# Performance work log

Hardware: AMD Instinct MI355X
Metric: run time of the kernel (lower is better)

Reference implementation:

```python
import jax, jax.numpy as jnp
import numpy as np

N_NODES = 10000
NEG_SLOPE = 0.2  # PyG GATv2Conv default


def gatv2(x, src, dst, Wl, bl, Wr, br, att, bias, n_nodes):
    """Single-head GATv2Conv (PyG defaults: heads=1, concat=True, self-loops added by caller)."""
    xl = x @ Wl + bl            # [N, dout] message source transform (lin_l)
    xr = x @ Wr + br            # [N, dout] target transform (lin_r)
    h = jax.nn.leaky_relu(xl[src] + xr[dst], NEG_SLOPE)   # [E, dout]
    e = h @ att                                            # [E] attention logits
    m = jax.ops.segment_max(e, dst, num_segments=n_nodes)  # per-target max
    ex = jnp.exp(e - m[dst])
    s = jax.ops.segment_sum(ex, dst, num_segments=n_nodes)
    alpha = ex / s[dst]                                    # segment softmax over incoming edges
    out = jax.ops.segment_sum(alpha[:, None] * xl[src], dst, num_segments=n_nodes)
    return out + bias


def _glorot(key, shape, scale=0.05):
    return jax.random.normal(key, shape, dtype=jnp.float32) * scale


def setup_inputs() -> dict:
    key = jax.random.key(0)
    ks = jax.random.split(key, 20)
    d_in, d0, d1 = 1000, 256, 128
    E = 320000
    x = jax.random.normal(ks[0], (N_NODES, d_in), dtype=jnp.float32)
    edge_index = jax.random.randint(ks[1], (2, E), 0, N_NODES, dtype=jnp.int64)
    return {
        "x": x,
        "edge_index": edge_index,
        # proj_in: d_in -> 256
        "Wpi": _glorot(ks[2], (d_in, d0)), "bpi": jnp.zeros((d0,), jnp.float32),
        # enc GATv2Conv 256 -> 128
        "Wl1": _glorot(ks[3], (d0, d1)), "bl1": jnp.zeros((d1,), jnp.float32),
        "Wr1": _glorot(ks[4], (d0, d1)), "br1": jnp.zeros((d1,), jnp.float32),
        "att1": _glorot(ks[5], (d1,)), "bias1": jnp.zeros((d1,), jnp.float32),
        # dec GATv2Conv 128 -> 256
        "Wl2": _glorot(ks[6], (d1, d0)), "bl2": jnp.zeros((d0,), jnp.float32),
        "Wr2": _glorot(ks[7], (d1, d0)), "br2": jnp.zeros((d0,), jnp.float32),
        "att2": _glorot(ks[8], (d0,)), "bias2": jnp.zeros((d0,), jnp.float32),
        # proj_out: 256 -> d_in
        "Wpo": _glorot(ks[9], (d0, d_in)), "bpo": jnp.zeros((d_in,), jnp.float32),
    }


def reference(x, edge_index, Wpi, bpi, Wl1, bl1, Wr1, br1, att1, bias1,
              Wl2, bl2, Wr2, br2, att2, bias2, Wpo, bpo):
    n = x.shape[0]
    # add self-loops (PyG GATv2Conv default add_self_loops=True)
    loops = jnp.arange(n, dtype=edge_index.dtype)
    src = jnp.concatenate([edge_index[0], loops])
    dst = jnp.concatenate([edge_index[1], loops])
    h = x @ Wpi + bpi
    z = gatv2(h, src, dst, Wl1, bl1, Wr1, br1, att1, bias1, n)
    d = gatv2(z, src, dst, Wl2, bl2, Wr2, br2, att2, bias2, n)
    x_hat = d @ Wpo + bpo
    return (x_hat, z)
```

## Files before the change

### kernel.cpp

```cpp
#include <hip/hip_runtime.h>
#include <math.h>

#define N_NODES 10000
#define MPAD    10112
#define D_IN    1000
#define KPAD_IN 1024
#define D0      256
#define D1      128
#define NPAD_OUT 1024
#define NEG_SLOPE 0.2f

typedef __attribute__((ext_vector_type(8))) short short8;
typedef __attribute__((ext_vector_type(4))) float f32x4;

__device__ __forceinline__ ushort f2bf(float f) {
  union { float f; unsigned u; } c; c.f = f;
  unsigned r = c.u + 0x7FFF + ((c.u >> 16) & 1);
  return (ushort)(r >> 16);
}
__device__ __forceinline__ float bf2f(ushort b) {
  union { unsigned u; float f; } c; c.u = ((unsigned)b) << 16;
  return c.f;
}


__global__ void count_kernel(const int* __restrict__ idx, int E, int n, int* __restrict__ counts) {
  int k = blockIdx.x * blockDim.x + threadIdx.x;
  int tot = E + n;
  if (k >= tot) return;
  int dst = (k < E) ? idx[E + k] : (k - E);
  atomicAdd(&counts[dst], 1);
}

__global__ void scan_kernel(const int* __restrict__ counts, int* __restrict__ offsets,
                            int* __restrict__ cursors, int n) {
  __shared__ int tsum[1024];
  int tid = threadIdx.x;
  int per = (n + 1023) / 1024;
  int start = tid * per;
  int end = start + per; if (end > n) end = n;
  int s = 0;
  for (int i = start; i < end; i++) s += counts[i];
  tsum[tid] = s;
  __syncthreads();
  for (int off = 1; off < 1024; off <<= 1) {
    int v = (tid >= off) ? tsum[tid - off] : 0;
    __syncthreads();
    if (tid >= off) tsum[tid] += v;
    __syncthreads();
  }
  int run = (tid == 0) ? 0 : tsum[tid - 1];
  for (int i = start; i < end; i++) {
    offsets[i] = run; cursors[i] = run;
    run += counts[i];
  }
  if (tid == 1023) offsets[n] = tsum[1023];
}

__global__ void scatter_kernel(const int* __restrict__ idx, int E, int n,
                               int* __restrict__ cursors, int* __restrict__ srcs) {
  int k = blockIdx.x * blockDim.x + threadIdx.x;
  int tot = E + n;
  if (k >= tot) return;
  int src, dst;
  if (k < E) { src = idx[k]; dst = idx[E + k]; }
  else       { src = k - E;  dst = src; }
  int pos = atomicAdd(&cursors[dst], 1);
  srcs[pos] = src;
}


__global__ void conv_x_kernel(const float* __restrict__ x, ushort* __restrict__ xb) {
  int idx = blockIdx.x * blockDim.x + threadIdx.x;
  int r = idx >> 8, k4 = (idx & 255) * 4;
  ushort4 o = {0, 0, 0, 0};
  if (r < N_NODES && k4 < D_IN) {
    float4 v = *(const float4*)(x + (size_t)r * D_IN + k4);
    o.x = f2bf(v.x); o.y = f2bf(v.y); o.z = f2bf(v.z); o.w = f2bf(v.w);
  }
  *(ushort4*)(xb + (size_t)idx * 4) = o;
}

#define T_WPI   (256 * 1024)
#define T_W1    (256 * 256)
#define T_W2    (512 * 128)
#define T_WPO   (1024 * 256)
#define OFF_W1  T_WPI
#define OFF_W2  (OFF_W1 + T_W1)
#define OFF_WPO (OFF_W2 + T_W2)
#define OFF_B   (OFF_WPO + T_WPO)
#define T_ALL   (OFF_B + 768)

__global__ void wprep_all(const float* __restrict__ Wpi,
                          const float* __restrict__ Wl1, const float* __restrict__ Wr1,
                          const float* __restrict__ Wl2, const float* __restrict__ Wr2,
                          const float* __restrict__ Wpo,
                          const float* __restrict__ bl1, const float* __restrict__ br1,
                          const float* __restrict__ bl2, const float* __restrict__ br2,
                          ushort* __restrict__ Wpi_t, ushort* __restrict__ W1cat,
                          ushort* __restrict__ W2cat, ushort* __restrict__ Wpo_t,
                          float* __restrict__ bcat1, float* __restrict__ bcat2) {
  int idx = blockIdx.x * 256 + threadIdx.x;
  if (idx >= T_ALL) return;
  if (idx < OFF_W1) {
    int n = idx >> 10, k = idx & 1023;
    Wpi_t[idx] = f2bf((k < 1000) ? Wpi[(size_t)k * 256 + n] : 0.f);
  } else if (idx < OFF_W2) {
    int q = idx - OFF_W1, n = q >> 8, k = q & 255;
    float v = (n < 128) ? Wl1[k * 128 + n] : Wr1[k * 128 + (n - 128)];
    W1cat[q] = f2bf(v);
  } else if (idx < OFF_WPO) {
    int q = idx - OFF_W2, n = q >> 7, k = q & 127;
    float v = (n < 256) ? Wl2[k * 256 + n] : Wr2[k * 256 + (n - 256)];
    W2cat[q] = f2bf(v);
  } else if (idx < OFF_B) {
    int q = idx - OFF_WPO, n = q >> 8, k = q & 255;
    Wpo_t[q] = f2bf((n < 1000) ? Wpo[(size_t)k * 1000 + n] : 0.f);
  } else {
    int q = idx - OFF_B;
    if (q < 128)      bcat1[q] = bl1[q];
    else if (q < 256) bcat1[q] = br1[q - 128];
    else if (q < 512) bcat2[q - 256] = bl2[q - 256];
    else              bcat2[q - 256] = br2[q - 512];
  }
}


template<int MODE>
__launch_bounds__(256)
__global__ void gemm_mfma(const ushort* __restrict__ A, int lda,
                          const ushort* __restrict__ Bt, int ldb,
                          const float* __restrict__ bias,
                          float* __restrict__ Cf, ushort* __restrict__ Cb, int ldp,
                          int M_valid, int N_valid, int K) {
  constexpr int BK = 32;
  __shared__ ushort As[128 * BK];
  __shared__ ushort Bs[128 * BK];
  const int tid  = threadIdx.x;
  const int lane = tid & 63, wave = tid >> 6;
  const int wr = wave >> 1, wc = wave & 1;
  const int bm = blockIdx.y * 128, bn = blockIdx.x * 128;
  const int r16 = lane & 15, kb = lane >> 4;

  f32x4 acc[4][4] = {};

  const int srow = tid >> 2;
  const int scol = (tid & 3) * 8;
  const ushort* Ag0 = A  + (size_t)(bm + srow) * lda + scol;
  const ushort* Ag1 = A  + (size_t)(bm + 64 + srow) * lda + scol;
  const ushort* Bg0 = Bt + (size_t)(bn + srow) * ldb + scol;
  const ushort* Bg1 = Bt + (size_t)(bn + 64 + srow) * ldb + scol;

  for (int k0 = 0; k0 < K; k0 += BK) {
    __builtin_amdgcn_global_load_lds((const __attribute__((address_space(1))) void*)(Ag0 + k0),
                                     (__attribute__((address_space(3))) void*)(As + tid * 8), 16, 0, 0);
    __builtin_amdgcn_global_load_lds((const __attribute__((address_space(1))) void*)(Ag1 + k0),
                                     (__attribute__((address_space(3))) void*)(As + 2048 + tid * 8), 16, 0, 0);
    __builtin_amdgcn_global_load_lds((const __attribute__((address_space(1))) void*)(Bg0 + k0),
                                     (__attribute__((address_space(3))) void*)(Bs + tid * 8), 16, 0, 0);
    __builtin_amdgcn_global_load_lds((const __attribute__((address_space(1))) void*)(Bg1 + k0),
                                     (__attribute__((address_space(3))) void*)(Bs + 2048 + tid * 8), 16, 0, 0);
    __syncthreads();

    short8 af[4], bfr[4];
    #pragma unroll
    for (int mi = 0; mi < 4; mi++)
      af[mi] = *(const short8*)(As + ((wr * 64 + mi * 16 + r16) * BK + kb * 8));
    #pragma unroll
    for (int ni = 0; ni < 4; ni++)
      bfr[ni] = *(const short8*)(Bs + ((wc * 64 + ni * 16 + r16) * BK + kb * 8));
    #pragma unroll
    for (int mi = 0; mi < 4; mi++)
      #pragma unroll
      for (int ni = 0; ni < 4; ni++)
        acc[mi][ni] = __builtin_amdgcn_mfma_f32_16x16x32_bf16(af[mi], bfr[ni], acc[mi][ni], 0, 0, 0);
    __syncthreads();
  }

  #pragma unroll
  for (int mi = 0; mi < 4; mi++) {
    const int row = bm + wr * 64 + mi * 16 + (lane >> 4) * 4;
    #pragma unroll
    for (int ni = 0; ni < 4; ni++) {
      const int col = bn + wc * 64 + ni * 16 + r16;
      const float bv = (col < N_valid) ? bias[col] : 0.f;
      #pragma unroll
      for (int r = 0; r < 4; r++) {
        const int gr = row + r;
        const float val = acc[mi][ni][r] + bv;
        if constexpr (MODE == 0) {
          if (gr < M_valid && col < N_valid) Cf[(size_t)gr * ldp + col] = val;
        } else if constexpr (MODE == 1) {
          Cb[(size_t)gr * ldp + col] = f2bf(gr < M_valid ? val : 0.f);
        } else {
          if (col < ldp) Cb[(size_t)gr * ldp + col] = f2bf(val);
          else           Cf[(size_t)gr * ldp + (col - ldp)] = val;
        }
      }
    }
  }
}


template<int D>
__launch_bounds__(256)
__global__ void gat_fused(const ushort* __restrict__ xlb, const float* __restrict__ xrf,
                          const float* __restrict__ att, const float* __restrict__ bias,
                          const int* __restrict__ offsets, const int* __restrict__ srcs,
                          float* __restrict__ out_f32, ushort* __restrict__ out_bf16,
                          int n_valid) {
  constexpr int EPL = D / 64;
  const int v    = blockIdx.x;
  const int tid  = threadIdx.x;
  const int lane = tid & 63;
  const int wave = tid >> 6;
  const int d0   = lane * EPL;

  if (v >= n_valid) {
    if (out_bf16 && tid < D) out_bf16[(size_t)v * D + tid] = 0;
    return;
  }

  __shared__ float m_s[4];
  __shared__ float s_s[4];
  __shared__ float buf[4][D];

  float rv[EPL], av[EPL], acc[EPL];
  #pragma unroll
  for (int d = 0; d < EPL; d++) {
    rv[d]  = xrf[(size_t)v * D + d0 + d];
    av[d]  = att[d0 + d];
    acc[d] = 0.f;
  }

  const int beg = offsets[v], end = offsets[v + 1];
  float m = -INFINITY, s = 0.f;

  int k = beg + wave;
  ushort xnxt[EPL];
  if (k < end) {
    const int u0 = srcs[k];
    if constexpr (EPL == 4) *(ushort4*)xnxt = *(const ushort4*)(xlb + (size_t)u0 * D + d0);
    else                    *(ushort2*)xnxt = *(const ushort2*)(xlb + (size_t)u0 * D + d0);
  }

  for (; k < end; k += 4) {
    ushort xcur[EPL];
    #pragma unroll
    for (int d = 0; d < EPL; d++) xcur[d] = xnxt[d];

    const int kn = k + 4;
    if (kn < end) {
      const int un = srcs[kn];
      if constexpr (EPL == 4) *(ushort4*)xnxt = *(const ushort4*)(xlb + (size_t)un * D + d0);
      else                    *(ushort2*)xnxt = *(const ushort2*)(xlb + (size_t)un * D + d0);
    }

    float xv[EPL], p = 0.f;
    #pragma unroll
    for (int d = 0; d < EPL; d++) {
      xv[d] = bf2f(xcur[d]);
      float t = xv[d] + rv[d];
      t = fmaxf(t, NEG_SLOPE * t);
      p = fmaf(t, av[d], p);
    }
    #pragma unroll
    for (int off = 32; off > 0; off >>= 1) p += __shfl_xor(p, off);

    const float m2   = fmaxf(m, p);
    const float cold = __expf(m - m2);
    const float w    = __expf(p - m2);
    s = s * cold + w;
    #pragma unroll
    for (int d = 0; d < EPL; d++) acc[d] = fmaf(acc[d], cold, w * xv[d]);
    m = m2;
  }

  if (lane == 0) m_s[wave] = m;
  __syncthreads();
  const float M = fmaxf(fmaxf(m_s[0], m_s[1]), fmaxf(m_s[2], m_s[3]));
  const float c = __expf(m - M);
  if (lane == 0) s_s[wave] = s * c;
  #pragma unroll
  for (int d = 0; d < EPL; d++) buf[wave][d0 + d] = acc[d] * c;
  __syncthreads();

  if (tid < D) {
    const float stot = s_s[0] + s_s[1] + s_s[2] + s_s[3];
    const float val = (buf[0][tid] + buf[1][tid] + buf[2][tid] + buf[3][tid]) / stot + bias[tid];
    if (out_f32)  out_f32[(size_t)v * D + tid] = val;
    if (out_bf16) out_bf16[(size_t)v * D + tid] = f2bf(val);
  }
}


extern "C" void kernel_launch(void* const* d_in, const int* in_sizes, int n_in,
                              void* d_out, int out_size, void* d_ws, size_t ws_size,
                              hipStream_t stream) {
  const float* x     = (const float*)d_in[0];
  const int*   eidx  = (const int*)d_in[1];
  const float* Wpi   = (const float*)d_in[2];
  const float* bpi   = (const float*)d_in[3];
  const float* Wl1   = (const float*)d_in[4];
  const float* bl1   = (const float*)d_in[5];
  const float* Wr1   = (const float*)d_in[6];
  const float* br1   = (const float*)d_in[7];
  const float* att1  = (const float*)d_in[8];
  const float* bias1 = (const float*)d_in[9];
  const float* Wl2   = (const float*)d_in[10];
  const float* bl2   = (const float*)d_in[11];
  const float* Wr2   = (const float*)d_in[12];
  const float* br2   = (const float*)d_in[13];
  const float* att2  = (const float*)d_in[14];
  const float* bias2 = (const float*)d_in[15];
  const float* Wpo   = (const float*)d_in[16];
  const float* bpo   = (const float*)d_in[17];

  const int E    = in_sizes[1] / 2;
  const int n    = N_NODES;
  const int Etot = E + n;

  float* out_xhat = (float*)d_out;
  float* out_z    = (float*)d_out + (size_t)N_NODES * D_IN;

  char* wp = (char*)d_ws;
  auto alloc = [&](size_t bytes) { char* p = wp; wp += (bytes + 255) & ~(size_t)255; return p; };
  char* regionA = (char*)alloc((size_t)MPAD * KPAD_IN * 2);
  ushort* hb_db = (ushort*)alloc((size_t)MPAD * D0 * 2);
  ushort* zb    = (ushort*)alloc((size_t)MPAD * D1 * 2);
  int* counts  = (int*)alloc((size_t)n * 4);
  int* offsets = (int*)alloc((size_t)(n + 1) * 4);
  int* cursors = (int*)alloc((size_t)n * 4);
  int* srcs    = (int*)alloc((size_t)Etot * 4);
  ushort* Wpi_t = (ushort*)alloc((size_t)T_WPI * 2);
  ushort* W1cat = (ushort*)alloc((size_t)T_W1 * 2);
  ushort* W2cat = (ushort*)alloc((size_t)T_W2 * 2);
  ushort* Wpo_t = (ushort*)alloc((size_t)T_WPO * 2);
  float*  bcat1 = (float*)alloc(256 * 4);
  float*  bcat2 = (float*)alloc(512 * 4);

  ushort* xb   = (ushort*)regionA;
  float*  xr1f = (float*)regionA;
  ushort* xl1b = (ushort*)(regionA + 8 * 1024 * 1024);
  float*  xr2f = (float*)regionA;
  ushort* xl2b = (ushort*)(regionA + 12 * 1024 * 1024);
  ushort* hb   = hb_db;
  ushort* db   = hb_db;

  hipMemsetAsync(counts, 0, (size_t)n * 4, stream);
  const int tb = 256;
  count_kernel<<<(Etot + tb - 1) / tb, tb, 0, stream>>>(eidx, E, n, counts);
  scan_kernel<<<1, 1024, 0, stream>>>(counts, offsets, cursors, n);
  scatter_kernel<<<(Etot + tb - 1) / tb, tb, 0, stream>>>(eidx, E, n, cursors, srcs);

  conv_x_kernel<<<MPAD, 256, 0, stream>>>(x, xb);
  wprep_all<<<(T_ALL + 255) / 256, 256, 0, stream>>>(
      Wpi, Wl1, Wr1, Wl2, Wr2, Wpo, bl1, br1, bl2, br2,
      Wpi_t, W1cat, W2cat, Wpo_t, bcat1, bcat2);

  gemm_mfma<1><<<dim3(D0 / 128, MPAD / 128), 256, 0, stream>>>(
      xb, KPAD_IN, Wpi_t, KPAD_IN, bpi, nullptr, hb, D0, N_NODES, D0, KPAD_IN);
  gemm_mfma<2><<<dim3(256 / 128, MPAD / 128), 256, 0, stream>>>(
      hb, D0, W1cat, D0, bcat1, xr1f, xl1b, D1, N_NODES, 256, D0);
  gat_fused<D1><<<MPAD, 256, 0, stream>>>(xl1b, xr1f, att1, bias1,
                                          offsets, srcs, out_z, zb, N_NODES);
  gemm_mfma<2><<<dim3(512 / 128, MPAD / 128), 256, 0, stream>>>(
      zb, D1, W2cat, D1, bcat2, xr2f, xl2b, D0, N_NODES, 512, D1);
  gat_fused<D0><<<MPAD, 256, 0, stream>>>(xl2b, xr2f, att2, bias2,
                                          offsets, srcs, nullptr, db, N_NODES);
  gemm_mfma<0><<<dim3(NPAD_OUT / 128, MPAD / 128), 256, 0, stream>>>(
      db, D0, Wpo_t, D0, bpo, out_xhat, nullptr, D_IN, N_NODES, D_IN, D0);
}
```

Before: 347.9 us.

## Fuse prep kernels, shrink GEMM tiles to 64x64, add lazy-rescale online softmax

```diff
diff --git a/kernel.cpp b/kernel.cpp
--- a/kernel.cpp
+++ b/kernel.cpp
@@ -70,17 +70,6 @@
 }
 
 
-__global__ void conv_x_kernel(const float* __restrict__ x, ushort* __restrict__ xb) {
-  int idx = blockIdx.x * blockDim.x + threadIdx.x;
-  int r = idx >> 8, k4 = (idx & 255) * 4;
-  ushort4 o = {0, 0, 0, 0};
-  if (r < N_NODES && k4 < D_IN) {
-    float4 v = *(const float4*)(x + (size_t)r * D_IN + k4);
-    o.x = f2bf(v.x); o.y = f2bf(v.y); o.z = f2bf(v.z); o.w = f2bf(v.w);
-  }
-  *(ushort4*)(xb + (size_t)idx * 4) = o;
-}
-
 #define T_WPI   (256 * 1024)
 #define T_W1    (256 * 256)
 #define T_W2    (512 * 128)
@@ -90,38 +79,55 @@
 #define OFF_WPO (OFF_W2 + T_W2)
 #define OFF_B   (OFF_WPO + T_WPO)
 #define T_ALL   (OFF_B + 768)
-
-__global__ void wprep_all(const float* __restrict__ Wpi,
-                          const float* __restrict__ Wl1, const float* __restrict__ Wr1,
-                          const float* __restrict__ Wl2, const float* __restrict__ Wr2,
-                          const float* __restrict__ Wpo,
-                          const float* __restrict__ bl1, const float* __restrict__ br1,
-                          const float* __restrict__ bl2, const float* __restrict__ br2,
-                          ushort* __restrict__ Wpi_t, ushort* __restrict__ W1cat,
-                          ushort* __restrict__ W2cat, ushort* __restrict__ Wpo_t,
-                          float* __restrict__ bcat1, float* __restrict__ bcat2) {
+#define CONV_T  (MPAD * 256)
+#define PREP_T  (CONV_T + T_ALL + N_NODES)
+
+__global__ void prep_all(const float* __restrict__ x, ushort* __restrict__ xb,
+                         const float* __restrict__ Wpi,
+                         const float* __restrict__ Wl1, const float* __restrict__ Wr1,
+                         const float* __restrict__ Wl2, const float* __restrict__ Wr2,
+                         const float* __restrict__ Wpo,
+                         const float* __restrict__ bl1, const float* __restrict__ br1,
+                         const float* __restrict__ bl2, const float* __restrict__ br2,
+                         ushort* __restrict__ Wpi_t, ushort* __restrict__ W1cat,
+                         ushort* __restrict__ W2cat, ushort* __restrict__ Wpo_t,
+                         float* __restrict__ bcat1, float* __restrict__ bcat2,
+                         int* __restrict__ counts) {
   int idx = blockIdx.x * 256 + threadIdx.x;
-  if (idx >= T_ALL) return;
-  if (idx < OFF_W1) {
-    int n = idx >> 10, k = idx & 1023;
-    Wpi_t[idx] = f2bf((k < 1000) ? Wpi[(size_t)k * 256 + n] : 0.f);
-  } else if (idx < OFF_W2) {
-    int q = idx - OFF_W1, n = q >> 8, k = q & 255;
+  if (idx < CONV_T) {
+    int r = idx >> 8, k4 = (idx & 255) * 4;
+    ushort4 o = {0, 0, 0, 0};
+    if (r < N_NODES && k4 < D_IN) {
+      float4 v = *(const float4*)(x + (size_t)r * D_IN + k4);
+      o.x = f2bf(v.x); o.y = f2bf(v.y); o.z = f2bf(v.z); o.w = f2bf(v.w);
+    }
+    *(ushort4*)(xb + (size_t)idx * 4) = o;
+    return;
+  }
+  int j = idx - CONV_T;
+  if (j < OFF_W1) {
+    int n = j >> 10, k = j & 1023;
+    Wpi_t[j] = f2bf((k < 1000) ? Wpi[(size_t)k * 256 + n] : 0.f);
+  } else if (j < OFF_W2) {
+    int q = j - OFF_W1, n = q >> 8, k = q & 255;
     float v = (n < 128) ? Wl1[k * 128 + n] : Wr1[k * 128 + (n - 128)];
     W1cat[q] = f2bf(v);
-  } else if (idx < OFF_WPO) {
-    int q = idx - OFF_W2, n = q >> 7, k = q & 127;
+  } else if (j < OFF_WPO) {
+    int q = j - OFF_W2, n = q >> 7, k = q & 127;
     float v = (n < 256) ? Wl2[k * 256 + n] : Wr2[k * 256 + (n - 256)];
     W2cat[q] = f2bf(v);
-  } else if (idx < OFF_B) {
-    int q = idx - OFF_WPO, n = q >> 8, k = q & 255;
+  } else if (j < OFF_B) {
+    int q = j - OFF_WPO, n = q >> 8, k = q & 255;
     Wpo_t[q] = f2bf((n < 1000) ? Wpo[(size_t)k * 1000 + n] : 0.f);
-  } else {
-    int q = idx - OFF_B;
+  } else if (j < T_ALL) {
+    int q = j - OFF_B;
     if (q < 128)      bcat1[q] = bl1[q];
     else if (q < 256) bcat1[q] = br1[q - 128];
     else if (q < 512) bcat2[q - 256] = bl2[q - 256];
     else              bcat2[q - 256] = br2[q - 512];
+  } else {
+    int q = j - T_ALL;
+    if (q < N_NODES) counts[q] = 0;
   }
 }
 
@@ -134,55 +140,49 @@
                           float* __restrict__ Cf, ushort* __restrict__ Cb, int ldp,
                           int M_valid, int N_valid, int K) {
   constexpr int BK = 32;
-  __shared__ ushort As[128 * BK];
-  __shared__ ushort Bs[128 * BK];
+  __shared__ ushort As[64 * BK];
+  __shared__ ushort Bs[64 * BK];
   const int tid  = threadIdx.x;
   const int lane = tid & 63, wave = tid >> 6;
   const int wr = wave >> 1, wc = wave & 1;
-  const int bm = blockIdx.y * 128, bn = blockIdx.x * 128;
+  const int bm = blockIdx.y * 64, bn = blockIdx.x * 64;
   const int r16 = lane & 15, kb = lane >> 4;
 
-  f32x4 acc[4][4] = {};
+  f32x4 acc[2][2] = {};
 
   const int srow = tid >> 2;
   const int scol = (tid & 3) * 8;
-  const ushort* Ag0 = A  + (size_t)(bm + srow) * lda + scol;
-  const ushort* Ag1 = A  + (size_t)(bm + 64 + srow) * lda + scol;
-  const ushort* Bg0 = Bt + (size_t)(bn + srow) * ldb + scol;
-  const ushort* Bg1 = Bt + (size_t)(bn + 64 + srow) * ldb + scol;
+  const ushort* Ag = A  + (size_t)(bm + srow) * lda + scol;
+  const ushort* Bg = Bt + (size_t)(bn + srow) * ldb + scol;
 
   for (int k0 = 0; k0 < K; k0 += BK) {
-    __builtin_amdgcn_global_load_lds((const __attribute__((address_space(1))) void*)(Ag0 + k0),
+    __builtin_amdgcn_global_load_lds((const __attribute__((address_space(1))) void*)(Ag + k0),
                                      (__attribute__((address_space(3))) void*)(As + tid * 8), 16, 0, 0);
-    __builtin_amdgcn_global_load_lds((const __attribute__((address_space(1))) void*)(Ag1 + k0),
-                                     (__attribute__((address_space(3))) void*)(As + 2048 + tid * 8), 16, 0, 0);
-    __builtin_amdgcn_global_load_lds((const __attribute__((address_space(1))) void*)(Bg0 + k0),
+    __builtin_amdgcn_global_load_lds((const __attribute__((address_space(1))) void*)(Bg + k0),
                                      (__attribute__((address_space(3))) void*)(Bs + tid * 8), 16, 0, 0);
-    __builtin_amdgcn_global_load_lds((const __attribute__((address_space(1))) void*)(Bg1 + k0),
-                                     (__attribute__((address_space(3))) void*)(Bs + 2048 + tid * 8), 16, 0, 0);
     __syncthreads();
 
-    short8 af[4], bfr[4];
-    #pragma unroll
-    for (int mi = 0; mi < 4; mi++)
-      af[mi] = *(const short8*)(As + ((wr * 64 + mi * 16 + r16) * BK + kb * 8));
-    #pragma unroll
-    for (int ni = 0; ni < 4; ni++)
-      bfr[ni] = *(const short8*)(Bs + ((wc * 64 + ni * 16 + r16) * BK + kb * 8));
-    #pragma unroll
-    for (int mi = 0; mi < 4; mi++)
+    short8 af[2], bfr[2];
+    #pragma unroll
+    for (int mi = 0; mi < 2; mi++)
+      af[mi] = *(const short8*)(As + ((wr * 32 + mi * 16 + r16) * BK + kb * 8));
+    #pragma unroll
+    for (int ni = 0; ni < 2; ni++)
+      bfr[ni] = *(const short8*)(Bs + ((wc * 32 + ni * 16 + r16) * BK + kb * 8));
+    #pragma unroll
+    for (int mi = 0; mi < 2; mi++)
       #pragma unroll
-      for (int ni = 0; ni < 4; ni++)
+      for (int ni = 0; ni < 2; ni++)
         acc[mi][ni] = __builtin_amdgcn_mfma_f32_16x16x32_bf16(af[mi], bfr[ni], acc[mi][ni], 0, 0, 0);
     __syncthreads();
   }
 
   #pragma unroll
-  for (int mi = 0; mi < 4; mi++) {
-    const int row = bm + wr * 64 + mi * 16 + (lane >> 4) * 4;
-    #pragma unroll
-    for (int ni = 0; ni < 4; ni++) {
-      const int col = bn + wc * 64 + ni * 16 + r16;
+  for (int mi = 0; mi < 2; mi++) {
+    const int row = bm + wr * 32 + mi * 16 + (lane >> 4) * 4;
+    #pragma unroll
+    for (int ni = 0; ni < 2; ni++) {
+      const int col = bn + wc * 32 + ni * 16 + r16;
       const float bv = (col < N_valid) ? bias[col] : 0.f;
       #pragma unroll
       for (int r = 0; r < 4; r++) {
@@ -267,13 +267,18 @@
     #pragma unroll
     for (int off = 32; off > 0; off >>= 1) p += __shfl_xor(p, off);
 
-    const float m2   = fmaxf(m, p);
-    const float cold = __expf(m - m2);
-    const float w    = __expf(p - m2);
-    s = s * cold + w;
-    #pragma unroll
-    for (int d = 0; d < EPL; d++) acc[d] = fmaf(acc[d], cold, w * xv[d]);
-    m = m2;
+    if (p <= m + 8.f) {
+      const float w = __expf(p - m);
+      s += w;
+      #pragma unroll
+      for (int d = 0; d < EPL; d++) acc[d] = fmaf(w, xv[d], acc[d]);
+    } else {
+      const float cold = __expf(m - p);
+      s = fmaf(s, cold, 1.f);
+      #pragma unroll
+      for (int d = 0; d < EPL; d++) acc[d] = fmaf(acc[d], cold, xv[d]);
+      m = p;
+    }
   }
 
   if (lane == 0) m_s[wave] = m;
@@ -347,27 +352,24 @@
   ushort* hb   = hb_db;
   ushort* db   = hb_db;
 
-  hipMemsetAsync(counts, 0, (size_t)n * 4, stream);
+  prep_all<<<(PREP_T + 255) / 256, 256, 0, stream>>>(
+      x, xb, Wpi, Wl1, Wr1, Wl2, Wr2, Wpo, bl1, br1, bl2, br2,
+      Wpi_t, W1cat, W2cat, Wpo_t, bcat1, bcat2, counts);
   const int tb = 256;
   count_kernel<<<(Etot + tb - 1) / tb, tb, 0, stream>>>(eidx, E, n, counts);
   scan_kernel<<<1, 1024, 0, stream>>>(counts, offsets, cursors, n);
   scatter_kernel<<<(Etot + tb - 1) / tb, tb, 0, stream>>>(eidx, E, n, cursors, srcs);
 
-  conv_x_kernel<<<MPAD, 256, 0, stream>>>(x, xb);
-  wprep_all<<<(T_ALL + 255) / 256, 256, 0, stream>>>(
-      Wpi, Wl1, Wr1, Wl2, Wr2, Wpo, bl1, br1, bl2, br2,
-      Wpi_t, W1cat, W2cat, Wpo_t, bcat1, bcat2);
-
-  gemm_mfma<1><<<dim3(D0 / 128, MPAD / 128), 256, 0, stream>>>(
+  gemm_mfma<1><<<dim3(D0 / 64, MPAD / 64), 256, 0, stream>>>(
       xb, KPAD_IN, Wpi_t, KPAD_IN, bpi, nullptr, hb, D0, N_NODES, D0, KPAD_IN);
-  gemm_mfma<2><<<dim3(256 / 128, MPAD / 128), 256, 0, stream>>>(
+  gemm_mfma<2><<<dim3(256 / 64, MPAD / 64), 256, 0, stream>>>(
       hb, D0, W1cat, D0, bcat1, xr1f, xl1b, D1, N_NODES, 256, D0);
   gat_fused<D1><<<MPAD, 256, 0, stream>>>(xl1b, xr1f, att1, bias1,
                                           offsets, srcs, out_z, zb, N_NODES);
-  gemm_mfma<2><<<dim3(512 / 128, MPAD / 128), 256, 0, stream>>>(
+  gemm_mfma<2><<<dim3(512 / 64, MPAD / 64), 256, 0, stream>>>(
       zb, D1, W2cat, D1, bcat2, xr2f, xl2b, D0, N_NODES, 512, D1);
   gat_fused<D0><<<MPAD, 256, 0, stream>>>(xl2b, xr2f, att2, bias2,
                                           offsets, srcs, nullptr, db, N_NODES);
-  gemm_mfma<0><<<dim3(NPAD_OUT / 128, MPAD / 128), 256, 0, stream>>>(
+  gemm_mfma<0><<<dim3(NPAD_OUT / 64, MPAD / 64), 256, 0, stream>>>(
       db, D0, Wpo_t, D0, bpo, out_xhat, nullptr, D_IN, N_NODES, D_IN, D0);
 }
```

Result: faster. 322.3 us (-7.4%).
